# Optimization experiments

Hardware: AMD Instinct MI355X
Metric: run time of the kernel (lower is better)

Reference implementation:

```python
import jax, jax.numpy as jnp
import numpy as np

NUM_BATCHES = 2


def _bn(x, gamma, beta, eps=1e-5):
    # training-mode BatchNorm1d over active-voxel rows (biased variance, as torch)
    mu = x.mean(axis=0)
    var = x.var(axis=0)
    return (x - mu) * jax.lax.rsqrt(var + eps) * gamma + beta


def setup_inputs() -> dict:
    rng = np.random.default_rng(0)
    B, Z, Y, X = 2, 8, 512, 512
    Cin, Cout, R = 64, 128, 16
    Yo, Xo = Y // 2, X // 2
    N = 200_000
    lin = np.sort(rng.choice(B * Z * Y * X, size=N, replace=False))
    b = lin // (Z * Y * X); r = lin % (Z * Y * X)
    z = r // (Y * X); r = r % (Y * X)
    y = r // X; x = r % X
    bz = b * Z + z
    # spconv rulebook for kernel (1,3,3), stride (1,2,2), pad (0,1,1)
    in_lists, out_lists = [], []
    for ky in range(3):
        for kx in range(3):
            oy2 = y + 1 - ky; ox2 = x + 1 - kx
            ok = ((oy2 >= 0) & (oy2 % 2 == 0) & (oy2 // 2 < Yo)
                  & (ox2 >= 0) & (ox2 % 2 == 0) & (ox2 // 2 < Xo))
            idx = np.nonzero(ok)[0]
            out_lin = (bz[idx] * Yo + oy2[idx] // 2) * Xo + ox2[idx] // 2
            in_lists.append(idx); out_lists.append(out_lin)
    all_out = np.concatenate(out_lists)
    uniq, inv = np.unique(all_out, return_inverse=True)
    M = uniq.shape[0]
    P = max(len(a) for a in in_lists)
    conv_in = np.full((9, P), N, dtype=np.int32)   # pad -> zero feature row
    conv_out = np.full((9, P), M, dtype=np.int32)  # pad -> dropped garbage row
    off = 0
    for k in range(9):
        L = len(in_lists[k])
        conv_in[k, :L] = in_lists[k]
        conv_out[k, :L] = inv[off:off + L]
        off += L
    # skip: kernel 1, stride (1,2,2) -> inputs with even (y,x); its output coords
    # are always present in the main conv output set (center tap ky=kx=1)
    skip_in = np.nonzero((y % 2 == 0) & (x % 2 == 0))[0].astype(np.int32)
    skip_lin = (bz[skip_in] * Yo + y[skip_in] // 2) * Xo + x[skip_in] // 2
    skip_out = np.searchsorted(uniq, skip_lin).astype(np.int32)
    batch_of_out = (uniq // (Z * Yo * Xo)).astype(np.int32)

    key = jax.random.key(0)
    ks = jax.random.split(key, 5)
    return dict(
        features=jax.random.normal(ks[0], (N, Cin), jnp.float32),
        W_conv=jax.random.normal(ks[1], (9, Cin, Cout), jnp.float32) / np.sqrt(9 * Cin),
        W_skip=jax.random.normal(ks[2], (Cin, Cout), jnp.float32) / np.sqrt(Cin),
        bn_gamma=jnp.ones((Cout,), jnp.float32), bn_beta=jnp.zeros((Cout,), jnp.float32),
        skip_bn_gamma=jnp.ones((Cout,), jnp.float32), skip_bn_beta=jnp.zeros((Cout,), jnp.float32),
        fc1=jax.random.normal(ks[3], (Cout, Cout // R), jnp.float32) / np.sqrt(Cout),
        fc2=jax.random.normal(ks[4], (Cout // R, Cout), jnp.float32) / np.sqrt(Cout // R),
        conv_in_idx=jnp.asarray(conv_in), conv_out_idx=jnp.asarray(conv_out),
        skip_in_idx=jnp.asarray(skip_in), skip_out_idx=jnp.asarray(skip_out),
        batch_of_out=jnp.asarray(batch_of_out))


def reference(features, W_conv, W_skip, bn_gamma, bn_beta, skip_bn_gamma,
              skip_bn_beta, fc1, fc2, conv_in_idx, conv_out_idx,
              skip_in_idx, skip_out_idx, batch_of_out):
    N, Cin = features.shape
    K, _, Cout = W_conv.shape
    M = batch_of_out.shape[0]
    feats_pad = jnp.concatenate([features, jnp.zeros((1, Cin), features.dtype)], 0)
    # sparse stride-2 conv: per-offset gather -> GEMM -> scatter-add
    out = jnp.zeros((M + 1, Cout), features.dtype)
    for k in range(K):  # 9 fixed kernel taps
        contrib = feats_pad[conv_in_idx[k]] @ W_conv[k]  # [P, Cout]
        out = out.at[conv_out_idx[k]].add(contrib)
    out = _bn(out[:M], bn_gamma, bn_beta)
    # 1x1 stride-2 skip branch, BN over its own active rows, scatter to out coords
    skip_feats = _bn(features[skip_in_idx] @ W_skip, skip_bn_gamma, skip_bn_beta)
    identity = jnp.zeros((M, Cout), features.dtype).at[skip_out_idx].set(skip_feats)
    # SparseGDSCA: per-batch global-avg descriptor -> SE channel attention
    sums = jax.ops.segment_sum(out, batch_of_out, num_segments=NUM_BATCHES)
    cnts = jax.ops.segment_sum(jnp.ones((M,), out.dtype), batch_of_out, num_segments=NUM_BATCHES)
    desc = sums / cnts[:, None]                              # [B, Cout]
    attn = jax.nn.sigmoid(jax.nn.relu(desc @ fc1) @ fc2)     # [B, Cout]
    out = out * attn[batch_of_out]
    return jax.nn.relu(out + identity)                        # [M, Cout]
```

## Files before the change

### kernel.cpp

```cpp
#include <hip/hip_runtime.h>

#define CIN 64
#define COUT 128
#define NC 64
#define NSB 32
#define LDT 132
#define SKB 256
#define SB 256

typedef __bf16 bf16x8 __attribute__((ext_vector_type(8)));
typedef __bf16 bf16x4 __attribute__((ext_vector_type(4)));
typedef float  f32x4  __attribute__((ext_vector_type(4)));

__global__ __launch_bounds__(256) void prep_kernel(
    const float* __restrict__ feats, __bf16* __restrict__ fb,
    const float* __restrict__ Wc, const float* __restrict__ Ws, __bf16* __restrict__ wf,
    const int* __restrict__ cin_idx, const int* __restrict__ cout_idx, int* __restrict__ tap_in,
    int* __restrict__ pat_arr,
    const int* __restrict__ sout, int* __restrict__ inv,
    const int* __restrict__ boo, int* __restrict__ msplit,
    int total8, int P, int cpb, int Ls, int N, int M,
    int nbA, int nbAB, int nbABC, int nbABCD)
{
    const int bid = blockIdx.x, t = threadIdx.x;
    if (bid < nbA) {
        const int i = bid * 256 + t;
        if (i >= total8) return;
        const int i8 = i * 8;
        const float4 x0 = *(const float4*)(feats + i8);
        const float4 x1 = *(const float4*)(feats + i8 + 4);
        bf16x8 v;
        v[0] = (__bf16)x0.x; v[1] = (__bf16)x0.y; v[2] = (__bf16)x0.z; v[3] = (__bf16)x0.w;
        v[4] = (__bf16)x1.x; v[5] = (__bf16)x1.y; v[6] = (__bf16)x1.z; v[7] = (__bf16)x1.w;
        *(bf16x8*)(fb + i8) = v;
    } else if (bid < nbAB) {
        const int id = (bid - nbA) * 256 + t;
        if (id >= 160 * 64) return;
        const int f = id >> 6, lane = id & 63;
        const float* W; int r;
        if (f < 144) { W = Wc + (size_t)(f >> 4) * CIN * COUT; r = f & 15; }
        else         { W = Ws;                                  r = f - 144; }
        const int c = r >> 1, s = r & 1;
        const int kbase = s * 32 + (lane >> 4) * 8;
        const int col = c * 16 + (lane & 15);
        bf16x8 v;
#pragma unroll
        for (int j = 0; j < 8; ++j) v[j] = (__bf16)W[(size_t)(kbase + j) * COUT + col];
        *(bf16x8*)(wf + ((size_t)f * 64 + lane) * 8) = v;
    } else if (bid < nbABC) {
        const int c = bid - nbAB;
        const int k = c / cpb;
        const int e = (c - k * cpb) * 256 + t;
        if (e >= P) return;
        const int oo = cout_idx[(size_t)k * P + e];
        if (oo < M) {
            tap_in[(size_t)k * M + oo] = cin_idx[(size_t)k * P + e];
            atomicOr(&pat_arr[oo], 1 << k);
        }
    } else if (bid < nbABCD) {
        const int i = (bid - nbABC) * 256 + t;
        if (i < Ls) inv[sout[i]] = i;
    } else {
        if (t < 64) fb[(size_t)N * CIN + t] = (__bf16)0.f;
        if (t == 0) {
            int lo = 0, hi = M;
            while (lo < hi) { const int mid = (lo + hi) >> 1; if (boo[mid] < 1) lo = mid + 1; else hi = mid; }
            msplit[0] = lo;
        }
    }
}

__global__ __launch_bounds__(256) void pat_kernel(
    const int* __restrict__ pat_arr, int* __restrict__ bh, int M, int rpb)
{
    __shared__ int lh[512];
    const int t = threadIdx.x, bid = blockIdx.x;
    lh[t] = 0; lh[t + 256] = 0;
    __syncthreads();
    const int mend = min((bid + 1) * rpb, M);
    for (int m = bid * rpb + t; m < mend; m += 256)
        atomicAdd(&lh[pat_arr[m]], 1);
    __syncthreads();
    bh[bid * 512 + t]       = lh[t];
    bh[bid * 512 + t + 256] = lh[t + 256];
}

__global__ __launch_bounds__(512) void scan_kernel(
    int* __restrict__ bh, int* __restrict__ rowid, int* __restrict__ ng_dev)
{
    __shared__ int buf[512];
    const int p = threadIdx.x;
    int total = 0;
    for (int b = 0; b < SB; ++b) total += bh[b * 512 + p];
    const int pc = (total + 15) & ~15;
    buf[p] = pc;
    __syncthreads();
    for (int off = 1; off < 512; off <<= 1) {
        const int v = (p >= off) ? buf[p - off] : 0;
        __syncthreads();
        buf[p] += v;
        __syncthreads();
    }
    int running = buf[p] - pc;
    if (p == 511) ng_dev[0] = buf[511] >> 4;
    for (int b = 0; b < SB; ++b) {
        const int c = bh[b * 512 + p];
        bh[b * 512 + p] = running;
        running += c;
    }
    for (int x = running; x < buf[p]; ++x) rowid[x] = -1;
}

__global__ __launch_bounds__(256) void scatter_kernel(
    const int* __restrict__ pat_arr, const int* __restrict__ bh,
    int* __restrict__ rowid, int* __restrict__ spat, int* __restrict__ boob,
    const int* __restrict__ boo, int M, int rpb)
{
    __shared__ int lcur[512];
    const int t = threadIdx.x, bid = blockIdx.x;
    lcur[t]       = bh[bid * 512 + t];
    lcur[t + 256] = bh[bid * 512 + t + 256];
    __syncthreads();
    const int mend = min((bid + 1) * rpb, M);
    for (int m = bid * rpb + t; m < mend; m += 256) {
        const int p = pat_arr[m];
        const int pos = atomicAdd(&lcur[p], 1);
        rowid[pos] = m;
        spat[pos] = p;
        boob[pos] = boo[m];
    }
}

__global__ __launch_bounds__(256, 4) void conv_mfma_kernel(
    const __bf16* __restrict__ fb,
    const __bf16* __restrict__ wf,
    const int* __restrict__ tap_in,
    const int* __restrict__ rowid,
    const int* __restrict__ spat,
    const int* __restrict__ boob,
    const int* __restrict__ ng_dev,
    const int* __restrict__ sin_idx,
    __bf16* __restrict__ raw,
    __bf16* __restrict__ G,
    float* __restrict__ zstats,
    int N, int M, int Ls)
{
    __shared__ float tile[4 * 16 * LDT];
    __shared__ float wred[3][4][128];
    const int t = threadIdx.x, lane = t & 63, wv = t >> 6;
    const int arow = lane & 15, apart = lane >> 4;

    if (blockIdx.x < SKB) {
        const __bf16* wk = wf + ((size_t)144 * 64 + lane) * 8;
        const bf16x8 b00 = *(const bf16x8*)(wk + (size_t)(wv * 4 + 0) * 512);
        const bf16x8 b01 = *(const bf16x8*)(wk + (size_t)(wv * 4 + 1) * 512);
        const bf16x8 b10 = *(const bf16x8*)(wk + (size_t)(wv * 4 + 2) * 512);
        const bf16x8 b11 = *(const bf16x8*)(wk + (size_t)(wv * 4 + 3) * 512);
        const int colA = wv * 32 + arow;
        const int colB = colA + 16;

        float s1A = 0.f, s2A = 0.f, s1B = 0.f, s2B = 0.f;
        const int ngroups = (Ls + 15) >> 4;
        for (int g = blockIdx.x; g < ngroups; g += SKB) {
            const int e0 = g * 16;
            const int ea = e0 + arow;
            const int ii = (ea < Ls) ? sin_idx[ea] : 0;
            const __bf16* fr = fb + (size_t)ii * CIN + apart * 8;
            const bf16x8 a0 = *(const bf16x8*)fr;
            const bf16x8 a1 = *(const bf16x8*)(fr + 32);

            f32x4 dA = {0.f,0.f,0.f,0.f};
            f32x4 dB = {0.f,0.f,0.f,0.f};
            dA = __builtin_amdgcn_mfma_f32_16x16x32_bf16(a0, b00, dA, 0, 0, 0);
            dA = __builtin_amdgcn_mfma_f32_16x16x32_bf16(a1, b01, dA, 0, 0, 0);
            dB = __builtin_amdgcn_mfma_f32_16x16x32_bf16(a0, b10, dB, 0, 0, 0);
            dB = __builtin_amdgcn_mfma_f32_16x16x32_bf16(a1, b11, dB, 0, 0, 0);

            const int er = e0 + apart * 4;
#pragma unroll
            for (int j = 0; j < 4; ++j) {
                if (er + j < Ls) {
                    const float vA = dA[j], vB = dB[j];
                    G[(size_t)(er + j) * COUT + colA] = (__bf16)vA;
                    G[(size_t)(er + j) * COUT + colB] = (__bf16)vB;
                    s1A += vA; s2A += vA * vA;
                    s1B += vB; s2B += vB * vB;
                }
            }
        }
        s1A += __shfl_xor(s1A, 16); s1A += __shfl_xor(s1A, 32);
        s2A += __shfl_xor(s2A, 16); s2A += __shfl_xor(s2A, 32);
        s1B += __shfl_xor(s1B, 16); s1B += __shfl_xor(s1B, 32);
        s2B += __shfl_xor(s2B, 16); s2B += __shfl_xor(s2B, 32);
        if (apart == 0) {
            wred[0][0][colA] = s1A; wred[0][0][colB] = s1B;
            wred[1][0][colA] = s2A; wred[1][0][colB] = s2B;
        }
        __syncthreads();
        float* bucket = zstats + NC * 384 + (size_t)(blockIdx.x & (NSB - 1)) * 256;
        if (t < 128) {
            atomicAdd(&bucket[t],       wred[0][0][t]);
            atomicAdd(&bucket[128 + t], wred[1][0][t]);
        }
        return;
    }

    const int ng = ng_dev[0];
    const int g = (blockIdx.x - SKB) * 4 + wv;
    const bool live = g < ng;
    const int m0 = g * 16;

    f32x4 D[8];
#pragma unroll
    for (int c = 0; c < 8; ++c) D[c] = (f32x4){0.f,0.f,0.f,0.f};

    int rid = -1, pattern = 0;
    if (live) {
        rid = rowid[m0 + arow];
        pattern = spat[m0];
    }

    for (int pk = pattern; pk; pk &= (pk - 1)) {
        const int k = __builtin_ctz(pk);
        const int vi = (rid >= 0) ? tap_in[(size_t)k * M + rid] : N;
        const __bf16* f0 = fb + (size_t)vi * CIN + apart * 8;
        const bf16x8 a0 = *(const bf16x8*)f0;
        const bf16x8 a1 = *(const bf16x8*)(f0 + 32);
        const __bf16* wb = wf + ((size_t)(k * 16) * 64 + lane) * 8;
#pragma unroll
        for (int c = 0; c < 8; ++c) {
            const bf16x8 b0 = *(const bf16x8*)(wb + (size_t)(c * 2 + 0) * 512);
            const bf16x8 b1 = *(const bf16x8*)(wb + (size_t)(c * 2 + 1) * 512);
            D[c] = __builtin_amdgcn_mfma_f32_16x16x32_bf16(a0, b0, D[c], 0, 0, 0);
            D[c] = __builtin_amdgcn_mfma_f32_16x16x32_bf16(a1, b1, D[c], 0, 0, 0);
        }
    }

    float ssum[8], sq[8], s0[8];
#pragma unroll
    for (int c = 0; c < 8; ++c) { ssum[c] = 0.f; sq[c] = 0.f; s0[c] = 0.f; }
    int4 bb = {1, 1, 1, 1};
    if (live) bb = *(const int4*)&boob[m0 + apart * 4];
#pragma unroll
    for (int c = 0; c < 8; ++c) {
        const float v0 = D[c][0], v1 = D[c][1], v2 = D[c][2], v3 = D[c][3];
        ssum[c] += v0 + v1 + v2 + v3;
        sq[c]   += v0*v0 + v1*v1 + v2*v2 + v3*v3;
        if (bb.x == 0) s0[c] += v0;
        if (bb.y == 0) s0[c] += v1;
        if (bb.z == 0) s0[c] += v2;
        if (bb.w == 0) s0[c] += v3;
    }

    float* T = tile + wv * (16 * LDT);
#pragma unroll
    for (int c = 0; c < 8; ++c)
#pragma unroll
        for (int j = 0; j < 4; ++j)
            T[(apart * 4 + j) * LDT + c * 16 + arow] = D[c][j];
    if (live) {
#pragma unroll
        for (int i = 0; i < 8; ++i) {
            const int r = i * 2 + (lane >> 5);
            const int c4 = (lane & 31) * 4;
            const f32x4 vv = *(const f32x4*)&T[r * LDT + c4];
            bf16x4 o;
            o[0] = (__bf16)vv[0]; o[1] = (__bf16)vv[1];
            o[2] = (__bf16)vv[2]; o[3] = (__bf16)vv[3];
            *(bf16x4*)&raw[(size_t)(m0 + r) * 128 + c4] = o;
        }
    }

#pragma unroll
    for (int c = 0; c < 8; ++c) {
        ssum[c] += __shfl_xor(ssum[c], 16); ssum[c] += __shfl_xor(ssum[c], 32);
        s0[c]   += __shfl_xor(s0[c], 16);   s0[c]   += __shfl_xor(s0[c], 32);
        sq[c]   += __shfl_xor(sq[c], 16);   sq[c]   += __shfl_xor(sq[c], 32);
    }
    if (apart == 0) {
#pragma unroll
        for (int c = 0; c < 8; ++c) {
            const int col = c * 16 + arow;
            wred[0][wv][col] = s0[c];
            wred[1][wv][col] = ssum[c] - s0[c];
            wred[2][wv][col] = sq[c];
        }
    }
    __syncthreads();
    float* bucket = zstats + (size_t)(blockIdx.x & (NC - 1)) * 384;
    if (t < 128) {
        atomicAdd(&bucket[t],       wred[0][0][t] + wred[0][1][t] + wred[0][2][t] + wred[0][3][t]);
        atomicAdd(&bucket[128 + t], wred[1][0][t] + wred[1][1][t] + wred[1][2][t] + wred[1][3][t]);
        atomicAdd(&bucket[256 + t], wred[2][0][t] + wred[2][1][t] + wred[2][2][t] + wred[2][3][t]);
    }
}

__global__ __launch_bounds__(128) void params_kernel(
    const float* __restrict__ zstats,
    const int* __restrict__ msplit_p,
    const float* __restrict__ gamma, const float* __restrict__ beta,
    const float* __restrict__ sgamma, const float* __restrict__ sbeta,
    const float* __restrict__ fc1, const float* __restrict__ fc2,
    float* __restrict__ scale, float* __restrict__ shift,
    float* __restrict__ sscale, float* __restrict__ sshift,
    float* __restrict__ attn,
    int Ls, int M)
{
    __shared__ float desc[2][COUT];
    __shared__ float hid[2][8];
    const int ch = threadIdx.x;

    float s0 = 0.f, s1 = 0.f, q = 0.f;
    for (int b = 0; b < NC; ++b) {
        const float* st = zstats + (size_t)b * 384;
        s0 += st[ch]; s1 += st[128 + ch]; q += st[256 + ch];
    }
    float ss = 0.f, sqk = 0.f;
    const float* sk = zstats + NC * 384;
    for (int b = 0; b < NSB; ++b) {
        ss  += sk[(size_t)b * 256 + ch];
        sqk += sk[(size_t)b * 256 + 128 + ch];
    }

    const float c0 = (float)msplit_p[0], c1 = (float)M - c0;
    const float Mf = (float)M;
    const float mu  = (s0 + s1) / Mf;
    const float var = q / Mf - mu * mu;
    const float rs  = rsqrtf(var + 1e-5f);
    const float sc  = rs * gamma[ch];
    const float sh  = beta[ch] - mu * sc;
    scale[ch] = sc;
    shift[ch] = sh;
    desc[0][ch] = (s0 / c0) * sc + sh;
    desc[1][ch] = (s1 / c1) * sc + sh;

    const float lsf  = (float)Ls;
    const float mus  = ss / lsf;
    const float vars = sqk / lsf - mus * mus;
    const float rss  = rsqrtf(vars + 1e-5f);
    const float ssc  = rss * sgamma[ch];
    sscale[ch] = ssc;
    sshift[ch] = sbeta[ch] - mus * ssc;

    __syncthreads();
    if (ch < 16) {
        const int b = ch >> 3, h = ch & 7;
        float a = 0.f;
        for (int c = 0; c < COUT; ++c) a += desc[b][c] * fc1[c * 8 + h];
        hid[b][h] = fmaxf(a, 0.f);
    }
    __syncthreads();
    for (int b = 0; b < 2; ++b) {
        float a = 0.f;
        for (int h = 0; h < 8; ++h) a += hid[b][h] * fc2[h * COUT + ch];
        attn[b * COUT + ch] = 1.f / (1.f + expf(-a));
    }
}

__global__ __launch_bounds__(256) void final_kernel(
    const __bf16* __restrict__ raw,
    const int* __restrict__ rowid,
    const int* __restrict__ boob,
    const int* __restrict__ ng_dev,
    float* __restrict__ out,
    const __bf16* __restrict__ G,
    const int* __restrict__ inv_skip,
    const float* __restrict__ scale, const float* __restrict__ shift,
    const float* __restrict__ sscale, const float* __restrict__ sshift,
    const float* __restrict__ attn)
{
    const int t  = threadIdx.x;
    const int c4 = (t & 31) * 4;
    const int rw = t >> 5;
    const float4 sc  = *(const float4*)&scale[c4];
    const float4 sh  = *(const float4*)&shift[c4];
    const float4 ssc = *(const float4*)&sscale[c4];
    const float4 ssh = *(const float4*)&sshift[c4];
    const float4 at0 = *(const float4*)&attn[c4];
    const float4 at1 = *(const float4*)&attn[COUT + c4];
    const int S = ng_dev[0] << 4;

    for (int s = blockIdx.x * 8 + rw; s < S; s += gridDim.x * 8) {
        const int rid = rowid[s];
        if (rid < 0) continue;
        const bf16x4 rv = *(const bf16x4*)&raw[(size_t)s * COUT + c4];
        const int b = boob[s];
        const int j = inv_skip[rid];
        const float4 av = b ? at1 : at0;
        float4 y;
        y.x = ((float)rv[0] * sc.x + sh.x) * av.x;
        y.y = ((float)rv[1] * sc.y + sh.y) * av.y;
        y.z = ((float)rv[2] * sc.z + sh.z) * av.z;
        y.w = ((float)rv[3] * sc.w + sh.w) * av.w;
        if (j >= 0) {
            const bf16x4 gg = *(const bf16x4*)&G[(size_t)j * COUT + c4];
            y.x += (float)gg[0] * ssc.x + ssh.x;
            y.y += (float)gg[1] * ssc.y + ssh.y;
            y.z += (float)gg[2] * ssc.z + ssh.z;
            y.w += (float)gg[3] * ssc.w + ssh.w;
        }
        y.x = y.x > 0.f ? y.x : 0.f;
        y.y = y.y > 0.f ? y.y : 0.f;
        y.z = y.z > 0.f ? y.z : 0.f;
        y.w = y.w > 0.f ? y.w : 0.f;
        *(float4*)&out[(size_t)rid * COUT + c4] = y;
    }
}

extern "C" void kernel_launch(void* const* d_in, const int* in_sizes, int n_in,
                              void* d_out, int out_size, void* d_ws, size_t ws_size,
                              hipStream_t stream)
{
    const float* feats  = (const float*)d_in[0];
    const float* Wc     = (const float*)d_in[1];
    const float* Wsk    = (const float*)d_in[2];
    const float* gamma  = (const float*)d_in[3];
    const float* beta   = (const float*)d_in[4];
    const float* sgamma = (const float*)d_in[5];
    const float* sbeta  = (const float*)d_in[6];
    const float* fc1    = (const float*)d_in[7];
    const float* fc2    = (const float*)d_in[8];
    const int* cin_idx  = (const int*)d_in[9];
    const int* cout_idx = (const int*)d_in[10];
    const int* sin_idx  = (const int*)d_in[11];
    const int* sout_idx = (const int*)d_in[12];
    const int* boo      = (const int*)d_in[13];

    const int N  = in_sizes[0] / CIN;
    const int P  = in_sizes[9] / 9;
    const int Ls = in_sizes[11];
    const int M  = in_sizes[13];
    const int maxS = ((M + 15) & ~15) + 512 * 16;
    const int maxG = maxS >> 4;
    const int rpb = (M + SB - 1) / SB;

    float* out = (float*)d_out;

    char* ws = (char*)d_ws;
    __bf16* fb = (__bf16*)ws;
    size_t off = (size_t)(N + 1) * CIN * sizeof(__bf16);
    off = (off + 255) & ~(size_t)255;
    __bf16* wfrag = (__bf16*)(ws + off);
    off += (size_t)160 * 64 * 8 * sizeof(__bf16);
    off = (off + 255) & ~(size_t)255;
    int* tap_in = (int*)(ws + off);
    off += (size_t)9 * M * sizeof(int);
    off = (off + 255) & ~(size_t)255;
    __bf16* G = (__bf16*)(ws + off);
    off += (size_t)Ls * COUT * sizeof(__bf16);
    off = (off + 255) & ~(size_t)255;
    int* inv_skip = (int*)(ws + off);
    off += (size_t)M * sizeof(int);
    off = (off + 255) & ~(size_t)255;
    int* pat_arr = (int*)(ws + off);
    off += (size_t)M * sizeof(int);
    off = (off + 255) & ~(size_t)255;
    int* rowid = (int*)(ws + off);
    off += (size_t)maxS * sizeof(int);
    int* spat = (int*)(ws + off);
    off += (size_t)maxS * sizeof(int);
    int* boob = (int*)(ws + off);
    off += (size_t)maxS * sizeof(int);
    off = (off + 255) & ~(size_t)255;
    __bf16* raw = (__bf16*)(ws + off);
    off += (size_t)maxS * COUT * sizeof(__bf16);
    off = (off + 255) & ~(size_t)255;
    int* bh = (int*)(ws + off);
    off += (size_t)SB * 512 * sizeof(int);
    int* ng_dev = (int*)(ws + off);
    off += 256;
    float* zstats = (float*)(ws + off);
    off += (size_t)(NC * 384 + NSB * 256) * sizeof(float);
    int* msplit = (int*)(ws + off);
    off += 256;
    float* params = (float*)(ws + off);
    float* scale = params, *shift = params + 128;
    float* sscale = params + 256, *sshift = params + 384, *attn = params + 512;

    hipMemsetAsync(zstats, 0, (size_t)(NC * 384 + NSB * 256) * sizeof(float), stream);
    hipMemsetAsync(inv_skip, 0xFF, (size_t)M * sizeof(int), stream);
    hipMemsetAsync(pat_arr, 0, (size_t)M * sizeof(int), stream);

    const int total8 = N * CIN / 8;
    const int nbA = (total8 + 255) / 256;
    const int nbB = (160 * 64 + 255) / 256;
    const int cpb = (P + 255) / 256;
    const int nbAB = nbA + nbB;
    const int nbABC = nbAB + 9 * cpb;
    const int nbABCD = nbABC + (Ls + 255) / 256;
    prep_kernel<<<nbABCD + 1, 256, 0, stream>>>(
        feats, fb, Wc, Wsk, wfrag, cin_idx, cout_idx, tap_in, pat_arr,
        sout_idx, inv_skip, boo, msplit,
        total8, P, cpb, Ls, N, M, nbA, nbAB, nbABC, nbABCD);

    pat_kernel<<<SB, 256, 0, stream>>>(pat_arr, bh, M, rpb);
    scan_kernel<<<1, 512, 0, stream>>>(bh, rowid, ng_dev);
    scatter_kernel<<<SB, 256, 0, stream>>>(pat_arr, bh, rowid, spat, boob, boo, M, rpb);

    conv_mfma_kernel<<<SKB + (maxG + 3) / 4, 256, 0, stream>>>(
        fb, wfrag, tap_in, rowid, spat, boob, ng_dev, sin_idx,
        raw, G, zstats, N, M, Ls);

    params_kernel<<<1, 128, 0, stream>>>(
        zstats, msplit, gamma, beta, sgamma, sbeta, fc1, fc2,
        scale, shift, sscale, sshift, attn, Ls, M);

    final_kernel<<<2048, 256, 0, stream>>>(
        raw, rowid, boob, ng_dev, out, G, inv_skip,
        scale, shift, sscale, sshift, attn);
}
```

Before: 212.2 us.

## Precompute compacted per-slot gather table and merge workspace memsets

The scatter kernel now writes a slot-major gather table holding the input row index for each active tap of each sorted output row. The conv kernel reads it with coalesced loads instead of a dependent rowid then tap_in[k*M+rid] lookup, which removes one level of indirect, scattered loads from the MFMA inner loop. The skip inverse map is shifted by one so a zero memset replaces the 0xFF fill, letting zstats, pat_arr and inv_skip be cleared with a single memset. In exchange the scatter kernel does extra writes into a 9*maxS table, and the single-block scan kernel now fills padding rows for every slot.

New measurement: 218.8 us. 1.03x slower.

```diff
diff --git a/kernel.cpp b/kernel.cpp
--- a/kernel.cpp
+++ b/kernel.cpp
@@ -59,7 +59,7 @@
         }
     } else if (bid < nbABCD) {
         const int i = (bid - nbABC) * 256 + t;
-        if (i < Ls) inv[sout[i]] = i;
+        if (i < Ls) inv[sout[i]] = i + 1;
     } else {
         if (t < 64) fb[(size_t)N * CIN + t] = (__bf16)0.f;
         if (t == 0) {
@@ -86,7 +86,8 @@
 }
 
 __global__ __launch_bounds__(512) void scan_kernel(
-    int* __restrict__ bh, int* __restrict__ rowid, int* __restrict__ ng_dev)
+    int* __restrict__ bh, int* __restrict__ rowid, int* __restrict__ gtab,
+    int* __restrict__ ng_dev, int N, int maxS)
 {
     __shared__ int buf[512];
     const int p = threadIdx.x;
@@ -108,13 +109,19 @@
         bh[b * 512 + p] = running;
         running += c;
     }
-    for (int x = running; x < buf[p]; ++x) rowid[x] = -1;
+    const int nslots = __builtin_popcount(p);
+    for (int x = running; x < buf[p]; ++x) {
+        rowid[x] = -1;
+        for (int s = 0; s < nslots; ++s) gtab[(size_t)s * maxS + x] = N;
+    }
 }
 
 __global__ __launch_bounds__(256) void scatter_kernel(
     const int* __restrict__ pat_arr, const int* __restrict__ bh,
+    const int* __restrict__ tap_in,
     int* __restrict__ rowid, int* __restrict__ spat, int* __restrict__ boob,
-    const int* __restrict__ boo, int M, int rpb)
+    int* __restrict__ gtab,
+    const int* __restrict__ boo, int M, int rpb, int maxS)
 {
     __shared__ int lcur[512];
     const int t = threadIdx.x, bid = blockIdx.x;
@@ -128,14 +135,19 @@
         rowid[pos] = m;
         spat[pos] = p;
         boob[pos] = boo[m];
+        int slot = 0;
+        for (int pk = p; pk; pk &= (pk - 1)) {
+            const int k = __builtin_ctz(pk);
+            gtab[(size_t)slot * maxS + pos] = tap_in[(size_t)k * M + m];
+            ++slot;
+        }
     }
 }
 
 __global__ __launch_bounds__(256, 4) void conv_mfma_kernel(
     const __bf16* __restrict__ fb,
     const __bf16* __restrict__ wf,
-    const int* __restrict__ tap_in,
-    const int* __restrict__ rowid,
+    const int* __restrict__ gtab,
     const int* __restrict__ spat,
     const int* __restrict__ boob,
     const int* __restrict__ ng_dev,
@@ -143,7 +155,7 @@
     __bf16* __restrict__ raw,
     __bf16* __restrict__ G,
     float* __restrict__ zstats,
-    int N, int M, int Ls)
+    int N, int M, int Ls, int maxS)
 {
     __shared__ float tile[4 * 16 * LDT];
     __shared__ float wred[3][4][128];
@@ -214,15 +226,13 @@
 #pragma unroll
     for (int c = 0; c < 8; ++c) D[c] = (f32x4){0.f,0.f,0.f,0.f};
 
-    int rid = -1, pattern = 0;
-    if (live) {
-        rid = rowid[m0 + arow];
-        pattern = spat[m0];
-    }
-
+    const int pattern = live ? spat[m0] : 0;
+
+    int slot = 0;
     for (int pk = pattern; pk; pk &= (pk - 1)) {
         const int k = __builtin_ctz(pk);
-        const int vi = (rid >= 0) ? tap_in[(size_t)k * M + rid] : N;
+        const int vi = gtab[(size_t)slot * maxS + m0 + arow];
+        ++slot;
         const __bf16* f0 = fb + (size_t)vi * CIN + apart * 8;
         const bf16x8 a0 = *(const bf16x8*)f0;
         const bf16x8 a1 = *(const bf16x8*)(f0 + 32);
@@ -392,8 +402,8 @@
         y.y = ((float)rv[1] * sc.y + sh.y) * av.y;
         y.z = ((float)rv[2] * sc.z + sh.z) * av.z;
         y.w = ((float)rv[3] * sc.w + sh.w) * av.w;
-        if (j >= 0) {
-            const bf16x4 gg = *(const bf16x4*)&G[(size_t)j * COUT + c4];
+        if (j > 0) {
+            const bf16x4 gg = *(const bf16x4*)&G[(size_t)(j - 1) * COUT + c4];
             y.x += (float)gg[0] * ssc.x + ssh.x;
             y.y += (float)gg[1] * ssc.y + ssh.y;
             y.z += (float)gg[2] * ssc.z + ssh.z;
@@ -449,12 +459,6 @@
     __bf16* G = (__bf16*)(ws + off);
     off += (size_t)Ls * COUT * sizeof(__bf16);
     off = (off + 255) & ~(size_t)255;
-    int* inv_skip = (int*)(ws + off);
-    off += (size_t)M * sizeof(int);
-    off = (off + 255) & ~(size_t)255;
-    int* pat_arr = (int*)(ws + off);
-    off += (size_t)M * sizeof(int);
-    off = (off + 255) & ~(size_t)255;
     int* rowid = (int*)(ws + off);
     off += (size_t)maxS * sizeof(int);
     int* spat = (int*)(ws + off);
@@ -462,6 +466,9 @@
     int* boob = (int*)(ws + off);
     off += (size_t)maxS * sizeof(int);
     off = (off + 255) & ~(size_t)255;
+    int* gtab = (int*)(ws + off);
+    off += (size_t)9 * maxS * sizeof(int);
+    off = (off + 255) & ~(size_t)255;
     __bf16* raw = (__bf16*)(ws + off);
     off += (size_t)maxS * COUT * sizeof(__bf16);
     off = (off + 255) & ~(size_t)255;
@@ -469,17 +476,21 @@
     off += (size_t)SB * 512 * sizeof(int);
     int* ng_dev = (int*)(ws + off);
     off += 256;
-    float* zstats = (float*)(ws + off);
-    off += (size_t)(NC * 384 + NSB * 256) * sizeof(float);
     int* msplit = (int*)(ws + off);
     off += 256;
     float* params = (float*)(ws + off);
     float* scale = params, *shift = params + 128;
     float* sscale = params + 256, *sshift = params + 384, *attn = params + 512;
-
-    hipMemsetAsync(zstats, 0, (size_t)(NC * 384 + NSB * 256) * sizeof(float), stream);
-    hipMemsetAsync(inv_skip, 0xFF, (size_t)M * sizeof(int), stream);
-    hipMemsetAsync(pat_arr, 0, (size_t)M * sizeof(int), stream);
+    off += 768 * sizeof(float);
+    off = (off + 255) & ~(size_t)255;
+    float* zstats = (float*)(ws + off);
+    size_t zoff = off + (size_t)(NC * 384 + NSB * 256) * sizeof(float);
+    int* pat_arr = (int*)(ws + zoff);
+    zoff += (size_t)M * sizeof(int);
+    int* inv_skip = (int*)(ws + zoff);
+    zoff += (size_t)M * sizeof(int);
+
+    hipMemsetAsync(zstats, 0, zoff - off, stream);
 
     const int total8 = N * CIN / 8;
     const int nbA = (total8 + 255) / 256;
@@ -494,12 +505,13 @@
         total8, P, cpb, Ls, N, M, nbA, nbAB, nbABC, nbABCD);
 
     pat_kernel<<<SB, 256, 0, stream>>>(pat_arr, bh, M, rpb);
-    scan_kernel<<<1, 512, 0, stream>>>(bh, rowid, ng_dev);
-    scatter_kernel<<<SB, 256, 0, stream>>>(pat_arr, bh, rowid, spat, boob, boo, M, rpb);
+    scan_kernel<<<1, 512, 0, stream>>>(bh, rowid, gtab, ng_dev, N, maxS);
+    scatter_kernel<<<SB, 256, 0, stream>>>(pat_arr, bh, tap_in, rowid, spat, boob,
+                                           gtab, boo, M, rpb, maxS);
 
     conv_mfma_kernel<<<SKB + (maxG + 3) / 4, 256, 0, stream>>>(
-        fb, wfrag, tap_in, rowid, spat, boob, ng_dev, sin_idx,
-        raw, G, zstats, N, M, Ls);
+        fb, wfrag, gtab, spat, boob, ng_dev, sin_idx,
+        raw, G, zstats, N, M, Ls, maxS);
 
     params_kernel<<<1, 128, 0, stream>>>(
         zstats, msplit, gamma, beta, sgamma, sbeta, fc1, fc2,
```
